# Kernel optimization log

Hardware: AMD Instinct MI355X
Metric: run time of the kernel (lower is better)

## Reference

```python
import jax, jax.numpy as jnp
import numpy as np

H = 16
D_MODEL = 1024
D_K = D_MODEL // H
SEQ = 2048
BATCH = 2


def setup_inputs() -> dict:
    key = jax.random.key(0)
    ks = jax.random.split(key, 11)
    s = 1.0 / np.sqrt(D_MODEL)
    inp = {
        "query": jax.random.normal(ks[0], (SEQ, BATCH, D_MODEL), jnp.float32),
        "key_": jax.random.normal(ks[1], (SEQ, BATCH, D_MODEL), jnp.float32),
        "value": jax.random.normal(ks[2], (SEQ, BATCH, D_MODEL), jnp.float32),
        "Wq": jax.random.uniform(ks[3], (D_MODEL, D_MODEL), jnp.float32, -s, s),
        "bq": jax.random.uniform(ks[4], (D_MODEL,), jnp.float32, -s, s),
        "Wk": jax.random.uniform(ks[5], (D_MODEL, D_MODEL), jnp.float32, -s, s),
        "bk": jax.random.uniform(ks[6], (D_MODEL,), jnp.float32, -s, s),
        "Wv": jax.random.uniform(ks[7], (D_MODEL, D_MODEL), jnp.float32, -s, s),
        "bv": jax.random.uniform(ks[8], (D_MODEL,), jnp.float32, -s, s),
        "Wo": jax.random.uniform(ks[9], (D_MODEL, D_MODEL), jnp.float32, -s, s),
        "bo": jax.random.uniform(ks[10], (D_MODEL,), jnp.float32, -s, s),
    }
    return inp


def _mha(query, key_, value, Wq, bq, Wk, bk, Wv, bv, Wo, bo):
    S, B, D = query.shape
    # torch Linear: x @ W.T + b; then view(S,B,h,dk).transpose(0,2) -> [h,B,S,dk]
    def proj(x, W, b):
        return jnp.transpose((x @ W.T + b).reshape(S, B, H, D_K), (2, 1, 0, 3))

    q = proj(query, Wq, bq)   # [h, b, S, dk]
    k = proj(key_, Wk, bk)
    v = proj(value, Wv, bv)

    scores = jnp.einsum("hbqd,hbkd->hbqk", q, k) / jnp.sqrt(
        jnp.asarray(D_K, q.dtype)
    )  # [h, b, S, S]
    p_attn = jax.nn.softmax(scores, axis=-1)  # dropout p=0.0 -> identity
    x = jnp.einsum("hbqk,hbkd->hbqd", p_attn, v)  # [h, b, S, dk]
    x = jnp.transpose(x, (2, 1, 0, 3)).reshape(S, B, D)  # back to [S, B, D]
    return x @ Wo.T + bo


def reference(query, key_, value, Wq, bq, Wk, bk, Wv, bv, Wo, bo):
    return _mha(query, key_, value, Wq, bq, Wk, bk, Wv, bv, Wo, bo)
```

## Files before the change

### kernel.cpp

```cpp
#include <hip/hip_runtime.h>

#define SEQ   2048
#define BATCH 2
#define DM    1024
#define NH    16
#define DKD   64
#define MROWS (SEQ*BATCH)

#define QSCALE 0.18033688011112042f

using bf16x8 = __attribute__((ext_vector_type(8))) __bf16;
using bf16x4 = __attribute__((ext_vector_type(4))) __bf16;
using bf16x2 = __attribute__((ext_vector_type(2))) __bf16;
using f32x4  = __attribute__((ext_vector_type(4))) float;

__device__ __forceinline__ void gld_lds16(const __bf16* g, __bf16* l) {
  __builtin_amdgcn_global_load_lds(
      (__attribute__((address_space(1))) void*)(g),
      (__attribute__((address_space(3))) void*)(l), 16, 0, 0);
}

__global__ __launch_bounds__(256) void cvt_all(
    const float* __restrict__ s0, const float* __restrict__ s1,
    const float* __restrict__ s2, const float* __restrict__ s3,
    const float* __restrict__ s4, const float* __restrict__ s5,
    const float* __restrict__ s6,
    __bf16* __restrict__ d0, __bf16* __restrict__ d1, __bf16* __restrict__ d2,
    __bf16* __restrict__ d3, __bf16* __restrict__ d4, __bf16* __restrict__ d5,
    __bf16* __restrict__ d6, int n_big, int n_small) {
  int y = blockIdx.y;
  const float* s; __bf16* d;
  switch (y) {
    case 0: s = s0; d = d0; break;
    case 1: s = s1; d = d1; break;
    case 2: s = s2; d = d2; break;
    case 3: s = s3; d = d3; break;
    case 4: s = s4; d = d4; break;
    case 5: s = s5; d = d5; break;
    default: s = s6; d = d6; break;
  }
  int n = (y < 3) ? n_big : n_small;
  int i = (blockIdx.x * 256 + threadIdx.x) * 8;
  if (i >= n) return;
  const float4* sp = (const float4*)(s + i);
  float4 a = sp[0], b = sp[1];
  bf16x8 v;
  v[0]=(__bf16)a.x; v[1]=(__bf16)a.y; v[2]=(__bf16)a.z; v[3]=(__bf16)a.w;
  v[4]=(__bf16)b.x; v[5]=(__bf16)b.y; v[6]=(__bf16)b.z; v[7]=(__bf16)b.w;
  *(bf16x8*)(d + i) = v;
}

__device__ __forceinline__ void gemm_core(const __bf16* __restrict__ A,
                                          const __bf16* __restrict__ Bt,
                                          __bf16* Ash, __bf16* Bsh,
                                          f32x4 acc[4][4], int m0, int n0) {
  const int K = DM;
  int tid = threadIdx.x;
  int lane = tid & 63, quad = lane >> 4, l16 = lane & 15, sw = l16 & 7;
  int w = tid >> 6;
  int wm = (w & 1) * 64, wn = (w >> 1) * 64;
  for (int k0 = 0; k0 < K; k0 += 64) {
    __syncthreads();
#pragma unroll
    for (int it = 0; it < 4; ++it) {
      int c   = tid + it * 256;
      int row = c >> 3, pp = c & 7;
      int ko  = (pp ^ (row & 7)) << 3;
      int base = (tid - lane + it * 256) * 8;
      gld_lds16(A  + (size_t)(m0 + row) * K + k0 + ko, Ash + base);
      gld_lds16(Bt + (size_t)(n0 + row) * K + k0 + ko, Bsh + base);
    }
    __syncthreads();
#pragma unroll
    for (int kk = 0; kk < 2; ++kk) {
      bf16x8 af[4], bfr[4];
#pragma unroll
      for (int mi = 0; mi < 4; mi++)
        af[mi] = *(const bf16x8*)&Ash[(wm + mi * 16 + l16) * 64 +
                                      (((kk * 4 + quad) ^ sw) << 3)];
#pragma unroll
      for (int ni = 0; ni < 4; ni++)
        bfr[ni] = *(const bf16x8*)&Bsh[(wn + ni * 16 + l16) * 64 +
                                       (((kk * 4 + quad) ^ sw) << 3)];
#pragma unroll
      for (int mi = 0; mi < 4; mi++)
#pragma unroll
        for (int ni = 0; ni < 4; ni++)
          acc[mi][ni] = __builtin_amdgcn_mfma_f32_16x16x32_bf16(
              af[mi], bfr[ni], acc[mi][ni], 0, 0, 0);
    }
  }
}

__global__ __launch_bounds__(256, 3) void gemm_qkv(
    const __bf16* __restrict__ Xq, const __bf16* __restrict__ Xk,
    const __bf16* __restrict__ Xv, const __bf16* __restrict__ Wqkv,
    const float* __restrict__ bqp, const float* __restrict__ bkp,
    const float* __restrict__ bvp,
    __bf16* __restrict__ Qb, __bf16* __restrict__ Kb, __bf16* __restrict__ Vt) {
  __shared__ __bf16 Ash[128 * 64], Bsh[128 * 64];
  __shared__ __bf16 Esh[4][16 * 72];
  int z = blockIdx.z;
  const __bf16* A   = (z == 0) ? Xq : (z == 1) ? Xk : Xv;
  const __bf16* Bt  = Wqkv + (size_t)z * (DM * DM);
  const float* bias = (z == 0) ? bqp : (z == 1) ? bkp : bvp;
  int m0 = blockIdx.y * 128, n0 = blockIdx.x * 128;
  f32x4 acc[4][4] = {};
  gemm_core(A, Bt, Ash, Bsh, acc, m0, n0);

  int tid = threadIdx.x, lane = tid & 63, quad = lane >> 4, l16 = lane & 15;
  int w = tid >> 6, wm = (w & 1) * 64, wn = (w >> 1) * 64;
  __bf16* E = Esh[w];
  int n_base = n0 + wn;
  int hh = n_base >> 6;
  float scale = (z == 0) ? QSCALE : 1.0f;
  float bb[4];
#pragma unroll
  for (int ni = 0; ni < 4; ni++) bb[ni] = bias[n_base + ni * 16 + l16] * scale;

  if (z == 2) {
#pragma unroll
    for (int ni = 0; ni < 4; ni++) {
#pragma unroll
      for (int mi = 0; mi < 4; mi++) {
        int s0 = mi * 8 + quad * 2;
        bf16x2 p0, p1;
        p0[0] = (__bf16)(acc[mi][ni][0] + bb[ni]);
        p0[1] = (__bf16)(acc[mi][ni][2] + bb[ni]);
        p1[0] = (__bf16)(acc[mi][ni][1] + bb[ni]);
        p1[1] = (__bf16)(acc[mi][ni][3] + bb[ni]);
        *(bf16x2*)&E[l16 * 72 + s0]      = p0;
        *(bf16x2*)&E[l16 * 72 + 32 + s0] = p1;
      }
      asm volatile("s_waitcnt lgkmcnt(0)" ::: "memory");
#pragma unroll
      for (int pass = 0; pass < 2; pass++) {
        int ddl = pass * 8 + (lane >> 3);
        int col = (lane & 7) * 8;
        bf16x8 v = *(const bf16x8*)&E[ddl * 72 + col];
        int b2 = col >> 5, sl = col & 31;
        int dd = ni * 16 + ddl;
        int sg = ((m0 + wm) >> 1) + sl;
        *(bf16x8*)&Vt[(((size_t)hh * BATCH + b2) * DKD + dd) * SEQ + sg] = v;
      }
      asm volatile("s_waitcnt lgkmcnt(0)" ::: "memory");
    }
  } else {
    __bf16* Out = (z == 0) ? Qb : Kb;
#pragma unroll
    for (int mi = 0; mi < 4; mi++) {
#pragma unroll
      for (int ni = 0; ni < 4; ni++)
#pragma unroll
        for (int r = 0; r < 4; r++)
          E[(quad * 4 + r) * 72 + ni * 16 + l16] =
              (__bf16)fmaf(acc[mi][ni][r], scale, bb[ni]);
      asm volatile("s_waitcnt lgkmcnt(0)" ::: "memory");
#pragma unroll
      for (int pass = 0; pass < 2; pass++) {
        int row16 = pass * 8 + (lane >> 3);
        int coll  = (lane & 7) * 8;
        bf16x8 v = *(const bf16x8*)&E[row16 * 72 + coll];
        int m = m0 + wm + mi * 16 + row16;
        int s = m >> 1, b2 = m & 1;
        *(bf16x8*)&Out[(((size_t)hh * BATCH + b2) * SEQ + s) * DKD + coll] = v;
      }
      asm volatile("s_waitcnt lgkmcnt(0)" ::: "memory");
    }
  }
}

__global__ __launch_bounds__(256, 3) void gemm_out(
    const __bf16* __restrict__ A, const __bf16* __restrict__ Bt,
    const float* __restrict__ bias, float* __restrict__ out) {
  __shared__ __bf16 Ash[64 * 64], Bsh[128 * 64];
  const int K = DM;
  int m0 = blockIdx.y * 64, n0 = blockIdx.x * 128;
  int tid = threadIdx.x;
  int lane = tid & 63, quad = lane >> 4, l16 = lane & 15, sw = l16 & 7;
  int w = tid >> 6;
  int wm = (w & 1) * 32, wn = (w >> 1) * 64;
  f32x4 acc[2][4] = {};
  for (int k0 = 0; k0 < K; k0 += 64) {
    __syncthreads();
#pragma unroll
    for (int it = 0; it < 2; ++it) {
      int c = tid + it * 256;
      int row = c >> 3, pp = c & 7;
      int ko = (pp ^ (row & 7)) << 3;
      gld_lds16(A + (size_t)(m0 + row) * K + k0 + ko,
                Ash + (tid - lane + it * 256) * 8);
    }
#pragma unroll
    for (int it = 0; it < 4; ++it) {
      int c = tid + it * 256;
      int row = c >> 3, pp = c & 7;
      int ko = (pp ^ (row & 7)) << 3;
      gld_lds16(Bt + (size_t)(n0 + row) * K + k0 + ko,
                Bsh + (tid - lane + it * 256) * 8);
    }
    __syncthreads();
#pragma unroll
    for (int kk = 0; kk < 2; ++kk) {
      bf16x8 af[2], bfr[4];
#pragma unroll
      for (int mi = 0; mi < 2; mi++)
        af[mi] = *(const bf16x8*)&Ash[(wm + mi * 16 + l16) * 64 +
                                      (((kk * 4 + quad) ^ sw) << 3)];
#pragma unroll
      for (int ni = 0; ni < 4; ni++)
        bfr[ni] = *(const bf16x8*)&Bsh[(wn + ni * 16 + l16) * 64 +
                                       (((kk * 4 + quad) ^ sw) << 3)];
#pragma unroll
      for (int mi = 0; mi < 2; mi++)
#pragma unroll
        for (int ni = 0; ni < 4; ni++)
          acc[mi][ni] = __builtin_amdgcn_mfma_f32_16x16x32_bf16(
              af[mi], bfr[ni], acc[mi][ni], 0, 0, 0);
    }
  }
#pragma unroll
  for (int ni = 0; ni < 4; ni++) {
    int n = n0 + wn + ni * 16 + l16;
    float bb = bias[n];
#pragma unroll
    for (int mi = 0; mi < 2; mi++) {
#pragma unroll
      for (int r = 0; r < 4; r++) {
        int m = m0 + wm + mi * 16 + quad * 4 + r;
        out[(size_t)m * DM + n] = acc[mi][ni][r] + bb;
      }
    }
  }
}

__global__ __launch_bounds__(512, 4) void flash_attn(
    const __bf16* __restrict__ Qg, const __bf16* __restrict__ Kg,
    const __bf16* __restrict__ Vtg, __bf16* __restrict__ Xa) {
  __shared__ __bf16 Ksh[2][64 * 64];
  __shared__ __bf16 Vsh[2][64 * 64];
  __shared__ __bf16 Psh[8][16 * 64];
  int tid = threadIdx.x, w = tid >> 6, lane = tid & 63;
  int quad = lane >> 4, l16 = lane & 15, sw = l16 & 7;
  int n = blockIdx.x;
  int hb = n & 31, qi = n >> 5;
  int h = hb >> 1, b = hb & 1, q0 = qi * 128;
  size_t hboff = ((size_t)h * BATCH + b) * SEQ * DKD;
  const __bf16* Qp = Qg + hboff;
  const __bf16* Kp = Kg + hboff;
  const __bf16* Vp = Vtg + hboff;
  __bf16* Pw = Psh[w];

  bf16x8 qf[2];
#pragma unroll
  for (int kk = 0; kk < 2; kk++)
    qf[kk] = *(const bf16x8*)(
        Qp + (size_t)(q0 + w * 16 + l16) * DKD + kk * 32 + quad * 8);

  f32x4 o[4] = {};
  float l_a = 0.f, l_b = 0.f;

  {
    int c = tid;
    int r = c >> 3, pp = c & 7;
    int off = (pp ^ (r & 7)) << 3;
    gld_lds16(Kp + (size_t)r * DKD + off, Ksh[0] + c * 8);
    gld_lds16(Vp + (size_t)r * SEQ + off, Vsh[0] + c * 8);
  }

  for (int t = 0; t < SEQ / 64; ++t) {
    __syncthreads();
    if (t + 1 < SEQ / 64) {
      int k0n = (t + 1) * 64, bn = (t + 1) & 1;
      int c = tid;
      int r = c >> 3, pp = c & 7;
      int off = (pp ^ (r & 7)) << 3;
      gld_lds16(Kp + (size_t)(k0n + r) * DKD + off, Ksh[bn] + c * 8);
      gld_lds16(Vp + (size_t)r * SEQ + k0n + off, Vsh[bn] + c * 8);
    }
    const __bf16* Kb_ = Ksh[t & 1];
    const __bf16* Vb_ = Vsh[t & 1];

    f32x4 sc[4];
    __builtin_amdgcn_s_setprio(1);
#pragma unroll
    for (int ji = 0; ji < 4; ji++) {
      int rr = ji * 16 + l16;
      bf16x8 kf0 = *(const bf16x8*)&Kb_[rr * 64 + ((quad ^ sw) << 3)];
      bf16x8 kf1 = *(const bf16x8*)&Kb_[rr * 64 + (((4 + quad) ^ sw) << 3)];
      f32x4 t2 = {0.f, 0.f, 0.f, 0.f};
      t2 = __builtin_amdgcn_mfma_f32_16x16x32_bf16(kf0, qf[0], t2, 0, 0, 0);
      t2 = __builtin_amdgcn_mfma_f32_16x16x32_bf16(kf1, qf[1], t2, 0, 0, 0);
      sc[ji] = t2;
    }
    __builtin_amdgcn_s_setprio(0);

#pragma unroll
    for (int ji = 0; ji < 4; ji++) {
      bf16x4 pk;
#pragma unroll
      for (int r = 0; r < 4; r++) {
        float pv = exp2f(sc[ji][r]);
        if (ji & 1) l_b += pv; else l_a += pv;
        pk[r] = (__bf16)pv;
      }
      *(bf16x4*)&Pw[l16 * 64 +
                    (((ji * 2 + (quad >> 1)) ^ sw) << 3) + ((quad & 1) << 2)] = pk;
    }

    __builtin_amdgcn_s_setprio(1);
#pragma unroll
    for (int kk = 0; kk < 2; kk++) {
      bf16x8 pa = *(const bf16x8*)&Pw[l16 * 64 + (((kk * 4 + quad) ^ sw) << 3)];
#pragma unroll
      for (int ni = 0; ni < 4; ni++) {
        int rr = ni * 16 + l16;
        bf16x8 vb = *(const bf16x8*)&Vb_[rr * 64 + (((kk * 4 + quad) ^ sw) << 3)];
        o[ni] = __builtin_amdgcn_mfma_f32_16x16x32_bf16(pa, vb, o[ni], 0, 0, 0);
      }
    }
    __builtin_amdgcn_s_setprio(0);
  }

  float l_ = l_a + l_b;
  l_ += __shfl_xor(l_, 16, 64);
  l_ += __shfl_xor(l_, 32, 64);
  l_ = 1.0f / l_;
#pragma unroll
  for (int r = 0; r < 4; r++) {
    float li = __shfl(l_, quad * 4 + r, 64);
    int q = q0 + w * 16 + quad * 4 + r;
#pragma unroll
    for (int ni = 0; ni < 4; ni++) {
      int d = ni * 16 + l16;
      Xa[((size_t)q * BATCH + b) * DM + h * DKD + d] =
          (__bf16)(o[ni][r] * li);
    }
  }
}

extern "C" void kernel_launch(void* const* d_in, const int* in_sizes, int n_in,
                              void* d_out, int out_size, void* d_ws,
                              size_t ws_size, hipStream_t stream) {
  (void)in_sizes; (void)n_in; (void)out_size; (void)ws_size;
  const float* query = (const float*)d_in[0];
  const float* key_  = (const float*)d_in[1];
  const float* value = (const float*)d_in[2];
  const float* Wq = (const float*)d_in[3];
  const float* bq = (const float*)d_in[4];
  const float* Wk = (const float*)d_in[5];
  const float* bk = (const float*)d_in[6];
  const float* Wv = (const float*)d_in[7];
  const float* bv = (const float*)d_in[8];
  const float* Wo = (const float*)d_in[9];
  const float* bo = (const float*)d_in[10];

  const size_t NX = (size_t)MROWS * DM;
  const size_t NW = (size_t)DM * DM;
  __bf16* p    = (__bf16*)d_ws;
  __bf16* Xq   = p; p += NX;
  __bf16* Xk   = p; p += NX;
  __bf16* Xv   = p; p += NX;
  __bf16* Wqkv = p; p += 3 * NW;
  __bf16* Wob  = p; p += NW;
  __bf16* Qb   = p; p += NX;
  __bf16* Kb   = p; p += NX;
  __bf16* Vt   = p; p += NX;
  __bf16* Xa   = Xq;

  cvt_all<<<dim3((unsigned)(NX / 2048), 7), 256, 0, stream>>>(
      query, key_, value, Wq, Wk, Wv, Wo,
      Xq, Xk, Xv, Wqkv, Wqkv + NW, Wqkv + 2 * NW, Wob, (int)NX, (int)NW);

  gemm_qkv<<<dim3(DM / 128, MROWS / 128, 3), 256, 0, stream>>>(
      Xq, Xk, Xv, Wqkv, bq, bk, bv, Qb, Kb, Vt);
  flash_attn<<<dim3(512), 512, 0, stream>>>(Qb, Kb, Vt, Xa);
  gemm_out<<<dim3(DM / 128, MROWS / 64), 256, 0, stream>>>(
      Xa, Wob, bo, (float*)d_out);
}
```

Baseline: 224.9 us.

## Rewrite flash attention with 32x32 MFMA tiles and register-resident P

The attention kernel moves from 16x16x32 to 32x32x16 bf16 MFMA tiles, with each of 4 waves handling 32 query rows instead of 8 waves handling 16. The P matrix is no longer round-tripped through LDS: exp results are packed with v_cvt_pk_bf16_f32 and rearranged with v_permlane32_swap so they feed the PV MFMA directly from registers. The goal is to remove LDS traffic for P, cut the number of MFMA issues, and raise data reuse per K/V tile load. In exchange each wave holds more accumulator registers and each workgroup has half as many waves to hide latency.

```diff
diff --git a/kernel.cpp b/kernel.cpp
--- a/kernel.cpp
+++ b/kernel.cpp
@@ -13,6 +13,7 @@
 using bf16x4 = __attribute__((ext_vector_type(4))) __bf16;
 using bf16x2 = __attribute__((ext_vector_type(2))) __bf16;
 using f32x4  = __attribute__((ext_vector_type(4))) float;
+using f32x16 = __attribute__((ext_vector_type(16))) float;
 
 __device__ __forceinline__ void gld_lds16(const __bf16* g, __bf16* l) {
   __builtin_amdgcn_global_load_lds(
@@ -234,34 +235,35 @@
   }
 }
 
-__global__ __launch_bounds__(512, 4) void flash_attn(
+__global__ __launch_bounds__(256, 2) void flash_attn(
     const __bf16* __restrict__ Qg, const __bf16* __restrict__ Kg,
     const __bf16* __restrict__ Vtg, __bf16* __restrict__ Xa) {
   __shared__ __bf16 Ksh[2][64 * 64];
   __shared__ __bf16 Vsh[2][64 * 64];
-  __shared__ __bf16 Psh[8][16 * 64];
   int tid = threadIdx.x, w = tid >> 6, lane = tid & 63;
-  int quad = lane >> 4, l16 = lane & 15, sw = l16 & 7;
+  int l32 = lane & 31, hf = lane >> 5;
   int n = blockIdx.x;
   int hb = n & 31, qi = n >> 5;
-  int h = hb >> 1, b = hb & 1, q0 = qi * 128;
-  size_t hboff = ((size_t)h * BATCH + b) * SEQ * DKD;
+  int hd = hb >> 1, b = hb & 1, q0 = qi * 128;
+  int qbase = q0 + w * 32;
+  size_t hboff = ((size_t)hd * BATCH + b) * SEQ * DKD;
   const __bf16* Qp = Qg + hboff;
   const __bf16* Kp = Kg + hboff;
   const __bf16* Vp = Vtg + hboff;
-  __bf16* Pw = Psh[w];
-
-  bf16x8 qf[2];
-#pragma unroll
-  for (int kk = 0; kk < 2; kk++)
-    qf[kk] = *(const bf16x8*)(
-        Qp + (size_t)(q0 + w * 16 + l16) * DKD + kk * 32 + quad * 8);
-
-  f32x4 o[4] = {};
-  float l_a = 0.f, l_b = 0.f;
-
-  {
-    int c = tid;
+
+  bf16x8 qf[4];
+#pragma unroll
+  for (int kd = 0; kd < 4; kd++)
+    qf[kd] = *(const bf16x8*)(
+        Qp + (size_t)(qbase + l32) * DKD + kd * 16 + hf * 8);
+
+  f32x16 o0 = {0,0,0,0,0,0,0,0,0,0,0,0,0,0,0,0};
+  f32x16 o1 = {0,0,0,0,0,0,0,0,0,0,0,0,0,0,0,0};
+  float l0 = 0.f, l1 = 0.f;
+
+#pragma unroll
+  for (int it = 0; it < 2; ++it) {
+    int c = tid + it * 256;
     int r = c >> 3, pp = c & 7;
     int off = (pp ^ (r & 7)) << 3;
     gld_lds16(Kp + (size_t)r * DKD + off, Ksh[0] + c * 8);
@@ -272,70 +274,78 @@
     __syncthreads();
     if (t + 1 < SEQ / 64) {
       int k0n = (t + 1) * 64, bn = (t + 1) & 1;
-      int c = tid;
-      int r = c >> 3, pp = c & 7;
-      int off = (pp ^ (r & 7)) << 3;
-      gld_lds16(Kp + (size_t)(k0n + r) * DKD + off, Ksh[bn] + c * 8);
-      gld_lds16(Vp + (size_t)r * SEQ + k0n + off, Vsh[bn] + c * 8);
+#pragma unroll
+      for (int it = 0; it < 2; ++it) {
+        int c = tid + it * 256;
+        int r = c >> 3, pp = c & 7;
+        int off = (pp ^ (r & 7)) << 3;
+        gld_lds16(Kp + (size_t)(k0n + r) * DKD + off, Ksh[bn] + c * 8);
+        gld_lds16(Vp + (size_t)r * SEQ + k0n + off, Vsh[bn] + c * 8);
+      }
     }
     const __bf16* Kb_ = Ksh[t & 1];
     const __bf16* Vb_ = Vsh[t & 1];
 
-    f32x4 sc[4];
-    __builtin_amdgcn_s_setprio(1);
-#pragma unroll
-    for (int ji = 0; ji < 4; ji++) {
-      int rr = ji * 16 + l16;
-      bf16x8 kf0 = *(const bf16x8*)&Kb_[rr * 64 + ((quad ^ sw) << 3)];
-      bf16x8 kf1 = *(const bf16x8*)&Kb_[rr * 64 + (((4 + quad) ^ sw) << 3)];
-      f32x4 t2 = {0.f, 0.f, 0.f, 0.f};
-      t2 = __builtin_amdgcn_mfma_f32_16x16x32_bf16(kf0, qf[0], t2, 0, 0, 0);
-      t2 = __builtin_amdgcn_mfma_f32_16x16x32_bf16(kf1, qf[1], t2, 0, 0, 0);
-      sc[ji] = t2;
-    }
-    __builtin_amdgcn_s_setprio(0);
-
-#pragma unroll
-    for (int ji = 0; ji < 4; ji++) {
-      bf16x4 pk;
-#pragma unroll
-      for (int r = 0; r < 4; r++) {
-        float pv = exp2f(sc[ji][r]);
-        if (ji & 1) l_b += pv; else l_a += pv;
-        pk[r] = (__bf16)pv;
-      }
-      *(bf16x4*)&Pw[l16 * 64 +
-                    (((ji * 2 + (quad >> 1)) ^ sw) << 3) + ((quad & 1) << 2)] = pk;
-    }
-
-    __builtin_amdgcn_s_setprio(1);
-#pragma unroll
-    for (int kk = 0; kk < 2; kk++) {
-      bf16x8 pa = *(const bf16x8*)&Pw[l16 * 64 + (((kk * 4 + quad) ^ sw) << 3)];
-#pragma unroll
-      for (int ni = 0; ni < 4; ni++) {
-        int rr = ni * 16 + l16;
-        bf16x8 vb = *(const bf16x8*)&Vb_[rr * 64 + (((kk * 4 + quad) ^ sw) << 3)];
-        o[ni] = __builtin_amdgcn_mfma_f32_16x16x32_bf16(pa, vb, o[ni], 0, 0, 0);
-      }
-    }
-    __builtin_amdgcn_s_setprio(0);
-  }
-
-  float l_ = l_a + l_b;
-  l_ += __shfl_xor(l_, 16, 64);
+#pragma unroll
+    for (int jt = 0; jt < 2; ++jt) {
+      int rk = jt * 32 + l32;
+      f32x16 s = {0,0,0,0,0,0,0,0,0,0,0,0,0,0,0,0};
+#pragma unroll
+      for (int kd = 0; kd < 4; kd++) {
+        bf16x8 kf = *(const bf16x8*)&Kb_[rk * 64 +
+                                         (((kd * 2 + hf) ^ (rk & 7)) << 3)];
+        s = __builtin_amdgcn_mfma_f32_32x32x16_bf16(kf, qf[kd], s, 0, 0, 0);
+      }
+      unsigned L[4][2];
+#pragma unroll
+      for (int bq = 0; bq < 4; bq++) {
+        float p0 = exp2f(s[4 * bq + 0]);
+        float p1 = exp2f(s[4 * bq + 1]);
+        float p2 = exp2f(s[4 * bq + 2]);
+        float p3 = exp2f(s[4 * bq + 3]);
+        l0 += p0 + p2;
+        l1 += p1 + p3;
+        asm("v_cvt_pk_bf16_f32 %0, %1, %2" : "=v"(L[bq][0]) : "v"(p0), "v"(p1));
+        asm("v_cvt_pk_bf16_f32 %0, %1, %2" : "=v"(L[bq][1]) : "v"(p2), "v"(p3));
+      }
+#pragma unroll
+      for (int kp = 0; kp < 2; kp++) {
+        unsigned a0 = L[2 * kp][0], b0 = L[2 * kp + 1][0];
+        unsigned a1 = L[2 * kp][1], b1 = L[2 * kp + 1][1];
+        asm("v_permlane32_swap_b32 %0, %1" : "+v"(a0), "+v"(b0));
+        asm("v_permlane32_swap_b32 %0, %1" : "+v"(a1), "+v"(b1));
+        unsigned pw[4] = {a0, a1, b0, b1};
+        bf16x8 pa;
+        __builtin_memcpy(&pa, pw, 16);
+        int ks = jt * 2 + kp;
+        {
+          int rv = l32;
+          bf16x8 vb = *(const bf16x8*)&Vb_[rv * 64 +
+                                           (((ks * 2 + hf) ^ (rv & 7)) << 3)];
+          o0 = __builtin_amdgcn_mfma_f32_32x32x16_bf16(pa, vb, o0, 0, 0, 0);
+        }
+        {
+          int rv = 32 + l32;
+          bf16x8 vb = *(const bf16x8*)&Vb_[rv * 64 +
+                                           (((ks * 2 + hf) ^ (rv & 7)) << 3)];
+          o1 = __builtin_amdgcn_mfma_f32_32x32x16_bf16(pa, vb, o1, 0, 0, 0);
+        }
+      }
+    }
+  }
+
+  float l_ = l0 + l1;
   l_ += __shfl_xor(l_, 32, 64);
-  l_ = 1.0f / l_;
-#pragma unroll
-  for (int r = 0; r < 4; r++) {
-    float li = __shfl(l_, quad * 4 + r, 64);
-    int q = q0 + w * 16 + quad * 4 + r;
-#pragma unroll
-    for (int ni = 0; ni < 4; ni++) {
-      int d = ni * 16 + l16;
-      Xa[((size_t)q * BATCH + b) * DM + h * DKD + d] =
-          (__bf16)(o[ni][r] * li);
-    }
+  float linv = 1.0f / l_;
+
+#pragma unroll
+  for (int r = 0; r < 16; ++r) {
+    int qrow = (r & 3) + 8 * (r >> 2) + 4 * hf;
+    float li = __shfl(linv, qrow, 64);
+    int q = qbase + qrow;
+    __bf16* dst = Xa + ((size_t)q * BATCH + b) * DM + hd * DKD;
+    dst[l32]      = (__bf16)(o0[r] * li);
+    dst[32 + l32] = (__bf16)(o1[r] * li);
   }
 }
 
@@ -374,7 +384,7 @@
 
   gemm_qkv<<<dim3(DM / 128, MROWS / 128, 3), 256, 0, stream>>>(
       Xq, Xk, Xv, Wqkv, bq, bk, bv, Qb, Kb, Vt);
-  flash_attn<<<dim3(512), 512, 0, stream>>>(Qb, Kb, Vt, Xa);
+  flash_attn<<<dim3(512), 256, 0, stream>>>(Qb, Kb, Vt, Xa);
   gemm_out<<<dim3(DM / 128, MROWS / 64), 256, 0, stream>>>(
       Xa, Wob, bo, (float*)d_out);
 }
```

Result: no change. 225.9 us (+0.5%).
